# Kernel tuning notes

Hardware: AMD Instinct MI355X
Metric: run time of the kernel (lower is better)

The kernel has to match this reference:

```python
import jax, jax.numpy as jnp
import numpy as np

TEMPERATURE = 0.2
LAMBDA_GAMMA = 0.5
LAMBDA_REG = 1e-4
LAMBDA_MARGIN = 0.8
NUM_USERS = 100000
NUM_ITEMS = 50000
EMBED_DIM = 64
BATCH = 8192


def setup_inputs() -> dict:
    key = jax.random.key(0)
    k1, k2, k3, k4, k5 = jax.random.split(key, 5)
    # Xavier-uniform-like scale for embedding tables
    bound = float(np.sqrt(6.0 / (NUM_USERS + EMBED_DIM)))
    user_table = jax.random.uniform(k1, (NUM_USERS, EMBED_DIM), jnp.float32, -bound, bound)
    bound_i = float(np.sqrt(6.0 / (NUM_ITEMS + EMBED_DIM)))
    item_table = jax.random.uniform(k2, (NUM_ITEMS, EMBED_DIM), jnp.float32, -bound_i, bound_i)
    user = jax.random.randint(k3, (BATCH,), 0, NUM_USERS, dtype=jnp.int64 if jax.config.jax_enable_x64 else jnp.int32)
    positive = jax.random.randint(k4, (BATCH,), 0, NUM_ITEMS, dtype=user.dtype)
    negative = jax.random.randint(k5, (BATCH,), 0, NUM_ITEMS, dtype=user.dtype)
    return {"user_table": user_table, "item_table": item_table,
            "user": user, "positive": positive, "negative": negative}


def _l2_normalize(x, eps=1e-12):
    # matches torch.nn.functional.normalize(dim=1)
    n = jnp.linalg.norm(x, axis=1, keepdims=True)
    return x / jnp.maximum(n, eps)


def _cscf_loss(e1, e2, temperature, margin):
    e1 = _l2_normalize(e1)  # [B, D]
    e2 = _l2_normalize(e2)  # [B, D]
    sim = jnp.sum(e1 * e2, axis=-1)  # [B]
    pos_score = jnp.exp(sim / temperature) + jnp.exp(jax.nn.relu(sim - margin) / temperature)
    # [B, B] score matrix: cross similarities plus self similarities
    total = jnp.matmul(e1, e2.T) + jnp.matmul(e1, e1.T)
    total = jnp.exp(total / temperature) + jnp.exp(jax.nn.relu(total - margin) / temperature)
    total = jnp.sum(total, axis=1)  # [B]
    loss = -jnp.log(pos_score / total + 1e-5)
    return jnp.mean(loss)


def _bpr_loss(u, p, n):
    pos = jnp.sum(u * p, axis=-1)
    neg = jnp.sum(u * n, axis=-1)
    return -jnp.mean(jax.nn.log_sigmoid(pos - neg))


def _reg_loss(u, p, n):
    b = u.shape[0]
    return 0.5 * (jnp.sum(u ** 2) + jnp.sum(p ** 2) + jnp.sum(n ** 2)) / b


def reference(user_table, item_table, user, positive, negative):
    ue = user_table[user]      # [B, D]
    pe = item_table[positive]  # [B, D]
    ne = item_table[negative]  # [B, D]
    bpr = _bpr_loss(ue, pe, ne)
    reg = LAMBDA_REG * _reg_loss(ue, pe, ne)
    na = LAMBDA_GAMMA * _cscf_loss(ue, pe, TEMPERATURE, LAMBDA_MARGIN)
    return (bpr, reg, na)
```

## Files before the change

kernel.cpp:

```cpp
#include <hip/hip_runtime.h>
#include <hip/hip_bf16.h>

#define BATCH 8192
#define DIM 64
#define TINV 5.0f
#define MARGIN 0.8f
#define SCALE5 7.21347520444f
#define EM4 0.01831563889f
#define LGAMMA 0.5f
#define LREG 1e-4f

typedef __attribute__((ext_vector_type(8))) short short8;
typedef __attribute__((ext_vector_type(4))) float float4v;

__device__ __forceinline__ unsigned short f2bf(float f) {
    unsigned int u = __builtin_bit_cast(unsigned int, f);
    unsigned int r = (u + 0x7fffu + ((u >> 16) & 1u)) >> 16;
    return (unsigned short)r;
}

__global__ __launch_bounds__(256) void phase1(
    const float* __restrict__ utab,
    const float* __restrict__ itab,
    const int* __restrict__ user, const int* __restrict__ posi,
    const int* __restrict__ negi,
    unsigned short* __restrict__ e1_out, unsigned short* __restrict__ g_out,
    float* __restrict__ pos_score, float* __restrict__ row_bpr,
    float* __restrict__ row_reg, float* __restrict__ total)
{
    const int tid  = blockIdx.x * 256 + threadIdx.x;
    if (tid < BATCH) total[tid] = 0.0f;

    const int lane = threadIdx.x & 63;
    const int wv   = tid >> 6;
    const int sub  = lane >> 4;
    const int l16  = lane & 15;
    const int r    = wv * 4 + sub;

    const int ui = user[r], pi = posi[r], ni = negi[r];
    const float4 u = *(const float4*)&utab[(size_t)ui * DIM + l16 * 4];
    const float4 p = *(const float4*)&itab[(size_t)pi * DIM + l16 * 4];
    const float4 n = *(const float4*)&itab[(size_t)ni * DIM + l16 * 4];

    float up = u.x*p.x + u.y*p.y + u.z*p.z + u.w*p.w;
    float un = u.x*n.x + u.y*n.y + u.z*n.z + u.w*n.w;
    float uu = u.x*u.x + u.y*u.y + u.z*u.z + u.w*u.w;
    float pp = p.x*p.x + p.y*p.y + p.z*p.z + p.w*p.w;
    float nn = n.x*n.x + n.y*n.y + n.z*n.z + n.w*n.w;
    #pragma unroll
    for (int off = 1; off < 16; off <<= 1) {
        up += __shfl_xor(up, off);
        un += __shfl_xor(un, off);
        uu += __shfl_xor(uu, off);
        pp += __shfl_xor(pp, off);
        nn += __shfl_xor(nn, off);
    }
    const float nu  = fmaxf(sqrtf(uu), 1e-12f);
    const float npn = fmaxf(sqrtf(pp), 1e-12f);
    const float ia  = 1.0f / nu;
    const float ib  = 1.0f / npn;
    const float sa  = SCALE5 * ia;

    union { unsigned short h[4]; uint2 v; } pe1, pg;
    pe1.h[0] = f2bf(u.x * sa); pe1.h[1] = f2bf(u.y * sa);
    pe1.h[2] = f2bf(u.z * sa); pe1.h[3] = f2bf(u.w * sa);
    pg.h[0]  = f2bf(u.x * ia + p.x * ib); pg.h[1] = f2bf(u.y * ia + p.y * ib);
    pg.h[2]  = f2bf(u.z * ia + p.z * ib); pg.h[3] = f2bf(u.w * ia + p.w * ib);
    *(uint2*)&e1_out[r * DIM + l16 * 4] = pe1.v;
    *(uint2*)&g_out[r * DIM + l16 * 4]  = pg.v;

    if (l16 == 0) {
        const float sim = up * (ia * ib);
        pos_score[r] = __expf(sim * TINV) + __expf(fmaxf(sim - MARGIN, 0.0f) * TINV);
        const float x = up - un;
        row_bpr[r] = fmaxf(-x, 0.0f) + __logf(1.0f + __expf(-fabsf(x)));
        row_reg[r] = uu + pp + nn;
    }
}

__global__ __launch_bounds__(256) void phase2(
    const unsigned short* __restrict__ e1,
    const unsigned short* __restrict__ g,
    float* __restrict__ total)
{
    const int w = threadIdx.x >> 6;
    const int lane = threadIdx.x & 63;
    const int r0 = blockIdx.x * 64;
    const int jslice = blockIdx.y;
    const int rowsel = lane & 15;
    const int kbase = (lane >> 4) * 8;

    short8 a[4][2];
    #pragma unroll
    for (int rt = 0; rt < 4; rt++)
        #pragma unroll
        for (int ks = 0; ks < 2; ks++)
            a[rt][ks] = *(const short8*)&e1[(r0 + rt * 16 + rowsel) * DIM + ks * 32 + kbase];

    float rowacc[4][4];
    #pragma unroll
    for (int rt = 0; rt < 4; rt++)
        #pragma unroll
        for (int q = 0; q < 4; q++) rowacc[rt][q] = 0.0f;

    for (int it = 0; it < 4; it++) {
        const int j0 = jslice * 1024 + it * 256 + w * 64;
        short8 b[4][2];
        #pragma unroll
        for (int ct = 0; ct < 4; ct++)
            #pragma unroll
            for (int ks = 0; ks < 2; ks++)
                b[ct][ks] = *(const short8*)&g[(j0 + ct * 16 + rowsel) * DIM + ks * 32 + kbase];

        #pragma unroll
        for (int rt = 0; rt < 4; rt++) {
            #pragma unroll
            for (int ct = 0; ct < 4; ct++) {
                float4v acc = {0.0f, 0.0f, 0.0f, 0.0f};
                acc = __builtin_amdgcn_mfma_f32_16x16x32_bf16(a[rt][0], b[ct][0], acc, 0, 0, 0);
                acc = __builtin_amdgcn_mfma_f32_16x16x32_bf16(a[rt][1], b[ct][1], acc, 0, 0, 0);
                #pragma unroll
                for (int q = 0; q < 4; q++) {
                    const float e = exp2f(acc[q]);
                    rowacc[rt][q] += e + fmaxf(e * EM4, 1.0f);
                }
            }
        }
    }

    #pragma unroll
    for (int off = 1; off < 16; off <<= 1)
        #pragma unroll
        for (int rt = 0; rt < 4; rt++)
            #pragma unroll
            for (int q = 0; q < 4; q++)
                rowacc[rt][q] += __shfl_xor(rowacc[rt][q], off);

    if ((lane & 15) == 0) {
        const int rquad = lane >> 4;
        #pragma unroll
        for (int rt = 0; rt < 4; rt++)
            #pragma unroll
            for (int q = 0; q < 4; q++)
                atomicAdd(&total[r0 + rt * 16 + rquad * 4 + q], rowacc[rt][q]);
    }
}

__global__ __launch_bounds__(1024) void phase3(
    const float* __restrict__ pos_score, const float* __restrict__ total,
    const float* __restrict__ row_bpr, const float* __restrict__ row_reg,
    float* __restrict__ out)
{
    __shared__ float rb[16], rr[16], rn[16];
    float sb = 0.0f, sr = 0.0f, sn = 0.0f;
    for (int i = threadIdx.x; i < BATCH; i += 1024) {
        sb += row_bpr[i];
        sr += row_reg[i];
        sn += -__logf(pos_score[i] / total[i] + 1e-5f);
    }
    #pragma unroll
    for (int off = 32; off; off >>= 1) {
        sb += __shfl_xor(sb, off);
        sr += __shfl_xor(sr, off);
        sn += __shfl_xor(sn, off);
    }
    const int wid = threadIdx.x >> 6;
    if ((threadIdx.x & 63) == 0) { rb[wid] = sb; rr[wid] = sr; rn[wid] = sn; }
    __syncthreads();
    if (threadIdx.x == 0) {
        float tb = 0.0f, tr = 0.0f, tn = 0.0f;
        #pragma unroll
        for (int i = 0; i < 16; i++) { tb += rb[i]; tr += rr[i]; tn += rn[i]; }
        out[0] = tb / (float)BATCH;
        out[1] = LREG * 0.5f * tr / (float)BATCH;
        out[2] = LGAMMA * (tn / (float)BATCH);
    }
}

extern "C" void kernel_launch(void* const* d_in, const int* in_sizes, int n_in,
                              void* d_out, int out_size, void* d_ws, size_t ws_size,
                              hipStream_t stream) {
    const float* utab = (const float*)d_in[0];
    const float* itab = (const float*)d_in[1];
    const int* user = (const int*)d_in[2];
    const int* posi = (const int*)d_in[3];
    const int* negi = (const int*)d_in[4];

    char* ws = (char*)d_ws;
    unsigned short* e1 = (unsigned short*)ws;
    unsigned short* g  = (unsigned short*)(ws + (size_t)BATCH * DIM * 2);
    float* pos_score = (float*)(ws + 2 * (size_t)BATCH * DIM * 2);
    float* total     = pos_score + BATCH;
    float* row_bpr   = total + BATCH;
    float* row_reg   = row_bpr + BATCH;

    phase1<<<512, 256, 0, stream>>>(utab, itab, user, posi, negi,
                                    e1, g, pos_score, row_bpr, row_reg, total);
    phase2<<<dim3(128, 8), 256, 0, stream>>>(e1, g, total);
    phase3<<<1, 1024, 0, stream>>>(pos_score, total, row_bpr, row_reg,
                                   (float*)d_out);
}
```

Measured before the change: 114.5 us.

## Fuse final reduction into phase2 via last-block atomic counters, drop phase3

Removes the single-block phase3 kernel launch. Phase1 now reduces the BPR and reg terms per block into partials, and phase2 uses per-stripe completion counters so the last block for each row stripe computes the contrastive log terms. A global done counter then lets the final block write the three outputs. This saves a launch and a serial 1024-thread pass over the batch, in exchange for extra atomics, fences and a nondeterministic float summation order.

```diff
diff --git a/kernel.cpp b/kernel.cpp
--- a/kernel.cpp
+++ b/kernel.cpp
@@ -4,9 +4,9 @@
 #define BATCH 8192
 #define DIM 64
 #define TINV 5.0f
-#define MARGIN 0.8f
 #define SCALE5 7.21347520444f
 #define EM4 0.01831563889f
+#define MARGIN 0.8f
 #define LGAMMA 0.5f
 #define LREG 1e-4f
 
@@ -25,17 +25,18 @@
     const int* __restrict__ user, const int* __restrict__ posi,
     const int* __restrict__ negi,
     unsigned short* __restrict__ e1_out, unsigned short* __restrict__ g_out,
-    float* __restrict__ pos_score, float* __restrict__ row_bpr,
-    float* __restrict__ row_reg, float* __restrict__ total)
+    float* __restrict__ pos_score, float* __restrict__ total,
+    float* __restrict__ bpr_part, float* __restrict__ reg_part,
+    unsigned int* __restrict__ misc )
 {
-    const int tid  = blockIdx.x * 256 + threadIdx.x;
+    const int tid = blockIdx.x * 256 + threadIdx.x;
     if (tid < BATCH) total[tid] = 0.0f;
+    else if (tid < BATCH + 132) misc[tid - BATCH] = 0u;
 
     const int lane = threadIdx.x & 63;
     const int wv   = tid >> 6;
-    const int sub  = lane >> 4;
     const int l16  = lane & 15;
-    const int r    = wv * 4 + sub;
+    const int r    = wv * 4 + (lane >> 4);
 
     const int ui = user[r], pi = posi[r], ni = negi[r];
     const float4 u = *(const float4*)&utab[(size_t)ui * DIM + l16 * 4];
@@ -55,11 +56,9 @@
         pp += __shfl_xor(pp, off);
         nn += __shfl_xor(nn, off);
     }
-    const float nu  = fmaxf(sqrtf(uu), 1e-12f);
-    const float npn = fmaxf(sqrtf(pp), 1e-12f);
-    const float ia  = 1.0f / nu;
-    const float ib  = 1.0f / npn;
-    const float sa  = SCALE5 * ia;
+    const float ia = 1.0f / fmaxf(sqrtf(uu), 1e-12f);
+    const float ib = 1.0f / fmaxf(sqrtf(pp), 1e-12f);
+    const float sa = SCALE5 * ia;
 
     union { unsigned short h[4]; uint2 v; } pe1, pg;
     pe1.h[0] = f2bf(u.x * sa); pe1.h[1] = f2bf(u.y * sa);
@@ -72,20 +71,37 @@
     if (l16 == 0) {
         const float sim = up * (ia * ib);
         pos_score[r] = __expf(sim * TINV) + __expf(fmaxf(sim - MARGIN, 0.0f) * TINV);
-        const float x = up - un;
-        row_bpr[r] = fmaxf(-x, 0.0f) + __logf(1.0f + __expf(-fabsf(x)));
-        row_reg[r] = uu + pp + nn;
+    }
+    const float x  = up - un;
+    float rb = fmaxf(-x, 0.0f) + __logf(1.0f + __expf(-fabsf(x)));
+    float rr = uu + pp + nn;
+    rb += __shfl_xor(rb, 16); rb += __shfl_xor(rb, 32);
+    rr += __shfl_xor(rr, 16); rr += __shfl_xor(rr, 32);
+    __shared__ float sb4[4], sr4[4];
+    const int w = threadIdx.x >> 6;
+    if (lane == 0) { sb4[w] = rb; sr4[w] = rr; }
+    __syncthreads();
+    if (threadIdx.x == 0) {
+        bpr_part[blockIdx.x] = sb4[0] + sb4[1] + sb4[2] + sb4[3];
+        reg_part[blockIdx.x] = sr4[0] + sr4[1] + sr4[2] + sr4[3];
     }
 }
 
 __global__ __launch_bounds__(256) void phase2(
     const unsigned short* __restrict__ e1,
     const unsigned short* __restrict__ g,
-    float* __restrict__ total)
+    float* __restrict__ total, const float* __restrict__ pos_score,
+    const float* __restrict__ bpr_part, const float* __restrict__ reg_part,
+    unsigned int* __restrict__ misc, float* __restrict__ out)
 {
+    unsigned int* cnt  = misc;
+    unsigned int* done = misc + 128;
+    float* scal = (float*)(misc + 129);
+
     const int w = threadIdx.x >> 6;
     const int lane = threadIdx.x & 63;
-    const int r0 = blockIdx.x * 64;
+    const int stripe = blockIdx.x;
+    const int r0 = stripe * 64;
     const int jslice = blockIdx.y;
     const int rowsel = lane & 15;
     const int kbase = (lane >> 4) * 8;
@@ -144,36 +160,42 @@
             for (int q = 0; q < 4; q++)
                 atomicAdd(&total[r0 + rt * 16 + rquad * 4 + q], rowacc[rt][q]);
     }
-}
-
-__global__ __launch_bounds__(1024) void phase3(
-    const float* __restrict__ pos_score, const float* __restrict__ total,
-    const float* __restrict__ row_bpr, const float* __restrict__ row_reg,
-    float* __restrict__ out)
-{
-    __shared__ float rb[16], rr[16], rn[16];
-    float sb = 0.0f, sr = 0.0f, sn = 0.0f;
-    for (int i = threadIdx.x; i < BATCH; i += 1024) {
-        sb += row_bpr[i];
-        sr += row_reg[i];
-        sn += -__logf(pos_score[i] / total[i] + 1e-5f);
-    }
-    #pragma unroll
-    for (int off = 32; off; off >>= 1) {
-        sb += __shfl_xor(sb, off);
-        sr += __shfl_xor(sr, off);
-        sn += __shfl_xor(sn, off);
-    }
-    const int wid = threadIdx.x >> 6;
-    if ((threadIdx.x & 63) == 0) { rb[wid] = sb; rr[wid] = sr; rn[wid] = sn; }
+
     __syncthreads();
+    __shared__ unsigned int lastf;
     if (threadIdx.x == 0) {
-        float tb = 0.0f, tr = 0.0f, tn = 0.0f;
-        #pragma unroll
-        for (int i = 0; i < 16; i++) { tb += rb[i]; tr += rr[i]; tn += rn[i]; }
-        out[0] = tb / (float)BATCH;
-        out[1] = LREG * 0.5f * tr / (float)BATCH;
-        out[2] = LGAMMA * (tn / (float)BATCH);
+        __threadfence();
+        lastf = (atomicAdd(&cnt[stripe], 1u) == 7u) ? 1u : 0u;
+    }
+    __syncthreads();
+    if (lastf && threadIdx.x < 64) {
+        __threadfence();
+        const int r = r0 + lane;
+        const float tot = atomicAdd(&total[r], 0.0f);
+        float v = -__logf(pos_score[r] / tot + 1e-5f);
+        #pragma unroll
+        for (int off = 1; off < 64; off <<= 1) v += __shfl_xor(v, off);
+        if (lane == 0) {
+            float sb = 0.0f, sr = 0.0f;
+            #pragma unroll
+            for (int k = 0; k < 4; k++) {
+                sb += bpr_part[stripe * 4 + k];
+                sr += reg_part[stripe * 4 + k];
+            }
+            atomicAdd(&scal[0], sb);
+            atomicAdd(&scal[1], sr);
+            atomicAdd(&scal[2], v);
+            __threadfence();
+            if (atomicAdd(done, 1u) == 127u) {
+                __threadfence();
+                const float tb = atomicAdd(&scal[0], 0.0f);
+                const float tr = atomicAdd(&scal[1], 0.0f);
+                const float tn = atomicAdd(&scal[2], 0.0f);
+                out[0] = tb / (float)BATCH;
+                out[1] = LREG * 0.5f * tr / (float)BATCH;
+                out[2] = LGAMMA * tn / (float)BATCH;
+            }
+        }
     }
 }
 
@@ -189,14 +211,16 @@
     char* ws = (char*)d_ws;
     unsigned short* e1 = (unsigned short*)ws;
     unsigned short* g  = (unsigned short*)(ws + (size_t)BATCH * DIM * 2);
-    float* pos_score = (float*)(ws + 2 * (size_t)BATCH * DIM * 2);
-    float* total     = pos_score + BATCH;
-    float* row_bpr   = total + BATCH;
-    float* row_reg   = row_bpr + BATCH;
+    float* pos_score   = (float*)(ws + 2 * (size_t)BATCH * DIM * 2);
+    float* total       = pos_score + BATCH;
+    float* bpr_part    = total + BATCH;
+    float* reg_part    = bpr_part + 512;
+    unsigned int* misc = (unsigned int*)(reg_part + 512);
 
     phase1<<<512, 256, 0, stream>>>(utab, itab, user, posi, negi,
-                                    e1, g, pos_score, row_bpr, row_reg, total);
-    phase2<<<dim3(128, 8), 256, 0, stream>>>(e1, g, total);
-    phase3<<<1, 1024, 0, stream>>>(pos_score, total, row_bpr, row_reg,
-                                   (float*)d_out);
-}
+                                    e1, g, pos_score, total,
+                                    bpr_part, reg_part, misc);
+    phase2<<<dim3(128, 8), 256, 0, stream>>>(e1, g, total, pos_score,
+                                             bpr_part, reg_part, misc,
+                                             (float*)d_out);
+}
```

New measurement: 125.6 us. 9.7% more time.

## Shrink phase2 to single-wave blocks with finer grid and simplify exp-sum expression

Applied to the files above, without the earlier changes.

Phase2 now uses 64-thread single-wavefront blocks, each covering 32 rows by 256 columns, on a 256x32 grid, with a launch-bounds occupancy hint. This replaces 256-thread blocks covering 64 rows by 1024 columns. The per-element score sum e + max(e*EM4, 1) is rewritten as max(e*CGT, e+1), which is algebraically equal and saves an instruction. Phase1 spreads each row over 32 lanes with float2 loads instead of 16 lanes with float4, doubling the grid. The finer phase2 grid raises parallelism but issues four times as many atomics on total, and each A-fragment load is reused across fewer columns.

```diff
diff --git a/kernel.cpp b/kernel.cpp
--- a/kernel.cpp
+++ b/kernel.cpp
@@ -4,9 +4,9 @@
 #define BATCH 8192
 #define DIM 64
 #define TINV 5.0f
+#define SCALE5 7.21347520444f
+#define CGT 1.01831563889f
 #define MARGIN 0.8f
-#define SCALE5 7.21347520444f
-#define EM4 0.01831563889f
 #define LGAMMA 0.5f
 #define LREG 1e-4f
 
@@ -28,48 +28,43 @@
     float* __restrict__ pos_score, float* __restrict__ row_bpr,
     float* __restrict__ row_reg, float* __restrict__ total)
 {
-    const int tid  = blockIdx.x * 256 + threadIdx.x;
+    const int tid = blockIdx.x * 256 + threadIdx.x;
     if (tid < BATCH) total[tid] = 0.0f;
 
     const int lane = threadIdx.x & 63;
     const int wv   = tid >> 6;
-    const int sub  = lane >> 4;
-    const int l16  = lane & 15;
-    const int r    = wv * 4 + sub;
+    const int l32  = lane & 31;
+    const int r    = wv * 2 + (lane >> 5);
 
     const int ui = user[r], pi = posi[r], ni = negi[r];
-    const float4 u = *(const float4*)&utab[(size_t)ui * DIM + l16 * 4];
-    const float4 p = *(const float4*)&itab[(size_t)pi * DIM + l16 * 4];
-    const float4 n = *(const float4*)&itab[(size_t)ni * DIM + l16 * 4];
+    const float2 u = *(const float2*)&utab[(size_t)ui * DIM + l32 * 2];
+    const float2 p = *(const float2*)&itab[(size_t)pi * DIM + l32 * 2];
+    const float2 n = *(const float2*)&itab[(size_t)ni * DIM + l32 * 2];
 
-    float up = u.x*p.x + u.y*p.y + u.z*p.z + u.w*p.w;
-    float un = u.x*n.x + u.y*n.y + u.z*n.z + u.w*n.w;
-    float uu = u.x*u.x + u.y*u.y + u.z*u.z + u.w*u.w;
-    float pp = p.x*p.x + p.y*p.y + p.z*p.z + p.w*p.w;
-    float nn = n.x*n.x + n.y*n.y + n.z*n.z + n.w*n.w;
+    float up = u.x*p.x + u.y*p.y;
+    float un = u.x*n.x + u.y*n.y;
+    float uu = u.x*u.x + u.y*u.y;
+    float pp = p.x*p.x + p.y*p.y;
+    float nn = n.x*n.x + n.y*n.y;
     #pragma unroll
-    for (int off = 1; off < 16; off <<= 1) {
+    for (int off = 1; off < 32; off <<= 1) {
         up += __shfl_xor(up, off);
         un += __shfl_xor(un, off);
         uu += __shfl_xor(uu, off);
         pp += __shfl_xor(pp, off);
         nn += __shfl_xor(nn, off);
     }
-    const float nu  = fmaxf(sqrtf(uu), 1e-12f);
-    const float npn = fmaxf(sqrtf(pp), 1e-12f);
-    const float ia  = 1.0f / nu;
-    const float ib  = 1.0f / npn;
-    const float sa  = SCALE5 * ia;
+    const float ia = 1.0f / fmaxf(sqrtf(uu), 1e-12f);
+    const float ib = 1.0f / fmaxf(sqrtf(pp), 1e-12f);
+    const float sa = SCALE5 * ia;
 
-    union { unsigned short h[4]; uint2 v; } pe1, pg;
+    union { unsigned short h[2]; unsigned int v; } pe1, pg;
     pe1.h[0] = f2bf(u.x * sa); pe1.h[1] = f2bf(u.y * sa);
-    pe1.h[2] = f2bf(u.z * sa); pe1.h[3] = f2bf(u.w * sa);
     pg.h[0]  = f2bf(u.x * ia + p.x * ib); pg.h[1] = f2bf(u.y * ia + p.y * ib);
-    pg.h[2]  = f2bf(u.z * ia + p.z * ib); pg.h[3] = f2bf(u.w * ia + p.w * ib);
-    *(uint2*)&e1_out[r * DIM + l16 * 4] = pe1.v;
-    *(uint2*)&g_out[r * DIM + l16 * 4]  = pg.v;
+    *(unsigned int*)&e1_out[r * DIM + l32 * 2] = pe1.v;
+    *(unsigned int*)&g_out[r * DIM + l32 * 2]  = pg.v;
 
-    if (l16 == 0) {
+    if (l32 == 0) {
         const float sim = up * (ia * ib);
         pos_score[r] = __expf(sim * TINV) + __expf(fmaxf(sim - MARGIN, 0.0f) * TINV);
         const float x = up - un;
@@ -78,33 +73,32 @@
     }
 }
 
-__global__ __launch_bounds__(256) void phase2(
+__global__ __launch_bounds__(64, 6) void phase2(
     const unsigned short* __restrict__ e1,
     const unsigned short* __restrict__ g,
     float* __restrict__ total)
 {
-    const int w = threadIdx.x >> 6;
-    const int lane = threadIdx.x & 63;
-    const int r0 = blockIdx.x * 64;
-    const int jslice = blockIdx.y;
+    const int lane = threadIdx.x;
+    const int r0 = blockIdx.x * 32;
+    const int jbase = blockIdx.y * 256;
     const int rowsel = lane & 15;
     const int kbase = (lane >> 4) * 8;
 
-    short8 a[4][2];
+    short8 a[2][2];
     #pragma unroll
-    for (int rt = 0; rt < 4; rt++)
+    for (int rt = 0; rt < 2; rt++)
         #pragma unroll
         for (int ks = 0; ks < 2; ks++)
             a[rt][ks] = *(const short8*)&e1[(r0 + rt * 16 + rowsel) * DIM + ks * 32 + kbase];
 
-    float rowacc[4][4];
+    float rowacc[2][4];
     #pragma unroll
-    for (int rt = 0; rt < 4; rt++)
+    for (int rt = 0; rt < 2; rt++)
         #pragma unroll
         for (int q = 0; q < 4; q++) rowacc[rt][q] = 0.0f;
 
     for (int it = 0; it < 4; it++) {
-        const int j0 = jslice * 1024 + it * 256 + w * 64;
+        const int j0 = jbase + it * 64;
         short8 b[4][2];
         #pragma unroll
         for (int ct = 0; ct < 4; ct++)
@@ -113,7 +107,7 @@
                 b[ct][ks] = *(const short8*)&g[(j0 + ct * 16 + rowsel) * DIM + ks * 32 + kbase];
 
         #pragma unroll
-        for (int rt = 0; rt < 4; rt++) {
+        for (int rt = 0; rt < 2; rt++) {
             #pragma unroll
             for (int ct = 0; ct < 4; ct++) {
                 float4v acc = {0.0f, 0.0f, 0.0f, 0.0f};
@@ -122,7 +116,7 @@
                 #pragma unroll
                 for (int q = 0; q < 4; q++) {
                     const float e = exp2f(acc[q]);
-                    rowacc[rt][q] += e + fmaxf(e * EM4, 1.0f);
+                    rowacc[rt][q] += fmaxf(e * CGT, e + 1.0f);
                 }
             }
         }
@@ -131,7 +125,7 @@
     #pragma unroll
     for (int off = 1; off < 16; off <<= 1)
         #pragma unroll
-        for (int rt = 0; rt < 4; rt++)
+        for (int rt = 0; rt < 2; rt++)
             #pragma unroll
             for (int q = 0; q < 4; q++)
                 rowacc[rt][q] += __shfl_xor(rowacc[rt][q], off);
@@ -139,7 +133,7 @@
     if ((lane & 15) == 0) {
         const int rquad = lane >> 4;
         #pragma unroll
-        for (int rt = 0; rt < 4; rt++)
+        for (int rt = 0; rt < 2; rt++)
             #pragma unroll
             for (int q = 0; q < 4; q++)
                 atomicAdd(&total[r0 + rt * 16 + rquad * 4 + q], rowacc[rt][q]);
@@ -189,14 +183,14 @@
     char* ws = (char*)d_ws;
     unsigned short* e1 = (unsigned short*)ws;
     unsigned short* g  = (unsigned short*)(ws + (size_t)BATCH * DIM * 2);
-    float* pos_score = (float*)(ws + 2 * (size_t)BATCH * DIM * 2);
-    float* total     = pos_score + BATCH;
-    float* row_bpr   = total + BATCH;
-    float* row_reg   = row_bpr + BATCH;
+    float* pos_score   = (float*)(ws + 2 * (size_t)BATCH * DIM * 2);
+    float* total       = pos_score + BATCH;
+    float* row_bpr     = total + BATCH;
+    float* row_reg     = row_bpr + BATCH;
 
-    phase1<<<512, 256, 0, stream>>>(utab, itab, user, posi, negi,
-                                    e1, g, pos_score, row_bpr, row_reg, total);
-    phase2<<<dim3(128, 8), 256, 0, stream>>>(e1, g, total);
+    phase1<<<1024, 256, 0, stream>>>(utab, itab, user, posi, negi,
+                                     e1, g, pos_score, row_bpr, row_reg, total);
+    phase2<<<dim3(256, 32), 64, 0, stream>>>(e1, g, total);
     phase3<<<1, 1024, 0, stream>>>(pos_score, total, row_bpr, row_reg,
                                    (float*)d_out);
 }
```

Result: slower. 124.2 us (+8.5%).

## Pre-swizzle G into MFMA fragment layout, simplify exp epilogue, parallelize final reduce

Applied to the files above, without the earlier changes.

Phase1 now writes the combined normalized matrix G in a tile-swizzled layout so each lane in phase2 loads its MFMA B fragments with fully contiguous 16-byte accesses. The point is to get coalesced loads in place of strided row gathers. The per-element epilogue is rewritten as a single max of e*(1+e^-4) and e+1, and uses the hardware exp2 intrinsic, which removes a multiply-add. Phase3 is spread across 8 blocks that combine their results with atomics into an output that phase1 zeroes, replacing the single-block loop.

```diff
diff --git a/kernel.cpp b/kernel.cpp
--- a/kernel.cpp
+++ b/kernel.cpp
@@ -4,9 +4,9 @@
 #define BATCH 8192
 #define DIM 64
 #define TINV 5.0f
+#define SCALE5 7.21347520444f
+#define CGT 1.01831563889f
 #define MARGIN 0.8f
-#define SCALE5 7.21347520444f
-#define EM4 0.01831563889f
 #define LGAMMA 0.5f
 #define LREG 1e-4f
 
@@ -24,18 +24,18 @@
     const float* __restrict__ itab,
     const int* __restrict__ user, const int* __restrict__ posi,
     const int* __restrict__ negi,
-    unsigned short* __restrict__ e1_out, unsigned short* __restrict__ g_out,
+    unsigned short* __restrict__ e1_out, unsigned short* __restrict__ g_sw,
     float* __restrict__ pos_score, float* __restrict__ row_bpr,
-    float* __restrict__ row_reg, float* __restrict__ total)
+    float* __restrict__ row_reg, float* __restrict__ total,
+    float* __restrict__ out)
 {
-    const int tid  = blockIdx.x * 256 + threadIdx.x;
+    const int tid = blockIdx.x * 256 + threadIdx.x;
     if (tid < BATCH) total[tid] = 0.0f;
+    if (tid < 3) out[tid] = 0.0f;
 
     const int lane = threadIdx.x & 63;
-    const int wv   = tid >> 6;
-    const int sub  = lane >> 4;
     const int l16  = lane & 15;
-    const int r    = wv * 4 + sub;
+    const int r    = (tid >> 6) * 4 + (lane >> 4);
 
     const int ui = user[r], pi = posi[r], ni = negi[r];
     const float4 u = *(const float4*)&utab[(size_t)ui * DIM + l16 * 4];
@@ -55,19 +55,25 @@
         pp += __shfl_xor(pp, off);
         nn += __shfl_xor(nn, off);
     }
-    const float nu  = fmaxf(sqrtf(uu), 1e-12f);
-    const float npn = fmaxf(sqrtf(pp), 1e-12f);
-    const float ia  = 1.0f / nu;
-    const float ib  = 1.0f / npn;
-    const float sa  = SCALE5 * ia;
-
-    union { unsigned short h[4]; uint2 v; } pe1, pg;
-    pe1.h[0] = f2bf(u.x * sa); pe1.h[1] = f2bf(u.y * sa);
-    pe1.h[2] = f2bf(u.z * sa); pe1.h[3] = f2bf(u.w * sa);
-    pg.h[0]  = f2bf(u.x * ia + p.x * ib); pg.h[1] = f2bf(u.y * ia + p.y * ib);
-    pg.h[2]  = f2bf(u.z * ia + p.z * ib); pg.h[3] = f2bf(u.w * ia + p.w * ib);
-    *(uint2*)&e1_out[r * DIM + l16 * 4] = pe1.v;
-    *(uint2*)&g_out[r * DIM + l16 * 4]  = pg.v;
+    const float ia = 1.0f / fmaxf(sqrtf(uu), 1e-12f);
+    const float ib = 1.0f / fmaxf(sqrtf(pp), 1e-12f);
+    const float sa = SCALE5 * ia;
+
+    union { unsigned short h[4]; uint2 v; } pa, pg;
+    pa.h[0] = f2bf(u.x * sa); pa.h[1] = f2bf(u.y * sa);
+    pa.h[2] = f2bf(u.z * sa); pa.h[3] = f2bf(u.w * sa);
+    pg.h[0] = f2bf(u.x * ia + p.x * ib); pg.h[1] = f2bf(u.y * ia + p.y * ib);
+    pg.h[2] = f2bf(u.z * ia + p.z * ib); pg.h[3] = f2bf(u.w * ia + p.w * ib);
+
+    *(uint2*)&e1_out[r * DIM + l16 * 4] = pa.v;
+
+    {
+        const int t = r >> 6, m = r & 63;
+        const int ct = m >> 4, rsel = m & 15;
+        const int ks = l16 >> 3, q = (l16 & 7) >> 1, half = l16 & 1;
+        const int off = t * 4096 + (ct * 2 + ks) * 512 + (q * 16 + rsel) * 8 + half * 4;
+        *(uint2*)&g_sw[off] = pg.v;
+    }
 
     if (l16 == 0) {
         const float sim = up * (ia * ib);
@@ -80,13 +86,12 @@
 
 __global__ __launch_bounds__(256) void phase2(
     const unsigned short* __restrict__ e1,
-    const unsigned short* __restrict__ g,
+    const unsigned short* __restrict__ g_sw,
     float* __restrict__ total)
 {
     const int w = threadIdx.x >> 6;
     const int lane = threadIdx.x & 63;
     const int r0 = blockIdx.x * 64;
-    const int jslice = blockIdx.y;
     const int rowsel = lane & 15;
     const int kbase = (lane >> 4) * 8;
 
@@ -103,14 +108,17 @@
         #pragma unroll
         for (int q = 0; q < 4; q++) rowacc[rt][q] = 0.0f;
 
+    const char* gbase = (const char*)g_sw + (size_t)lane * 16;
+
     for (int it = 0; it < 4; it++) {
-        const int j0 = jslice * 1024 + it * 256 + w * 64;
+        const int t = blockIdx.y * 16 + w * 4 + it;
+        const char* bp = gbase + (size_t)t * 8192;
         short8 b[4][2];
         #pragma unroll
         for (int ct = 0; ct < 4; ct++)
             #pragma unroll
             for (int ks = 0; ks < 2; ks++)
-                b[ct][ks] = *(const short8*)&g[(j0 + ct * 16 + rowsel) * DIM + ks * 32 + kbase];
+                b[ct][ks] = *(const short8*)(bp + (ct * 2 + ks) * 1024);
 
         #pragma unroll
         for (int rt = 0; rt < 4; rt++) {
@@ -121,8 +129,8 @@
                 acc = __builtin_amdgcn_mfma_f32_16x16x32_bf16(a[rt][1], b[ct][1], acc, 0, 0, 0);
                 #pragma unroll
                 for (int q = 0; q < 4; q++) {
-                    const float e = exp2f(acc[q]);
-                    rowacc[rt][q] += e + fmaxf(e * EM4, 1.0f);
+                    const float e = __builtin_amdgcn_exp2f(acc[q]);
+                    rowacc[rt][q] += fmaxf(e * CGT, e + 1.0f);
                 }
             }
         }
@@ -151,29 +159,27 @@
     const float* __restrict__ row_bpr, const float* __restrict__ row_reg,
     float* __restrict__ out)
 {
-    __shared__ float rb[16], rr[16], rn[16];
-    float sb = 0.0f, sr = 0.0f, sn = 0.0f;
-    for (int i = threadIdx.x; i < BATCH; i += 1024) {
-        sb += row_bpr[i];
-        sr += row_reg[i];
-        sn += -__logf(pos_score[i] / total[i] + 1e-5f);
-    }
+    const int i = blockIdx.x * 1024 + threadIdx.x;
+    float sb = row_bpr[i];
+    float sr = row_reg[i];
+    float sn = -__logf(pos_score[i] / total[i] + 1e-5f);
     #pragma unroll
     for (int off = 32; off; off >>= 1) {
         sb += __shfl_xor(sb, off);
         sr += __shfl_xor(sr, off);
         sn += __shfl_xor(sn, off);
     }
+    __shared__ float rb[16], rr[16], rn[16];
     const int wid = threadIdx.x >> 6;
     if ((threadIdx.x & 63) == 0) { rb[wid] = sb; rr[wid] = sr; rn[wid] = sn; }
     __syncthreads();
     if (threadIdx.x == 0) {
         float tb = 0.0f, tr = 0.0f, tn = 0.0f;
         #pragma unroll
-        for (int i = 0; i < 16; i++) { tb += rb[i]; tr += rr[i]; tn += rn[i]; }
-        out[0] = tb / (float)BATCH;
-        out[1] = LREG * 0.5f * tr / (float)BATCH;
-        out[2] = LGAMMA * (tn / (float)BATCH);
+        for (int k = 0; k < 16; k++) { tb += rb[k]; tr += rr[k]; tn += rn[k]; }
+        atomicAdd(&out[0], tb / (float)BATCH);
+        atomicAdd(&out[1], LREG * 0.5f * tr / (float)BATCH);
+        atomicAdd(&out[2], LGAMMA * tn / (float)BATCH);
     }
 }
 
@@ -187,16 +193,17 @@
     const int* negi = (const int*)d_in[4];
 
     char* ws = (char*)d_ws;
-    unsigned short* e1 = (unsigned short*)ws;
-    unsigned short* g  = (unsigned short*)(ws + (size_t)BATCH * DIM * 2);
-    float* pos_score = (float*)(ws + 2 * (size_t)BATCH * DIM * 2);
-    float* total     = pos_score + BATCH;
-    float* row_bpr   = total + BATCH;
-    float* row_reg   = row_bpr + BATCH;
+    unsigned short* e1   = (unsigned short*)ws;
+    unsigned short* g_sw = (unsigned short*)(ws + (size_t)BATCH * DIM * 2);
+    float* pos_score     = (float*)(ws + 2 * (size_t)BATCH * DIM * 2);
+    float* total         = pos_score + BATCH;
+    float* row_bpr       = total + BATCH;
+    float* row_reg       = row_bpr + BATCH;
 
     phase1<<<512, 256, 0, stream>>>(utab, itab, user, posi, negi,
-                                    e1, g, pos_score, row_bpr, row_reg, total);
-    phase2<<<dim3(128, 8), 256, 0, stream>>>(e1, g, total);
-    phase3<<<1, 1024, 0, stream>>>(pos_score, total, row_bpr, row_reg,
+                                    e1, g_sw, pos_score, row_bpr, row_reg,
+                                    total, (float*)d_out);
+    phase2<<<dim3(128, 8), 256, 0, stream>>>(e1, g_sw, total);
+    phase3<<<8, 1024, 0, stream>>>(pos_score, total, row_bpr, row_reg,
                                    (float*)d_out);
 }
```

Result: faster. 103.7 us (-9.5%).
